# Kernel tuning notes

Hardware: AMD Instinct MI355X
Metric: run time of the kernel (lower is better)

## Reference

```python
import jax, jax.numpy as jnp
import numpy as np

EPS = 1e-5

def setup_inputs() -> dict:
    key = jax.random.key(0)
    ks = jax.random.split(key, 10)
    B, N, D = 1, 20000, 256
    E, H = 320000, 8
    s = 1.0 / np.sqrt(D)
    return {
        "node_embeddings": jax.random.normal(ks[0], (B, N, D), jnp.float32),
        "edge_index": jax.random.randint(ks[1], (2, E), 0, N, jnp.int32),
        "edge_weights": jax.random.uniform(ks[2], (E,), jnp.float32),
        "Wq": jax.random.normal(ks[3], (D, D), jnp.float32) * s,
        "Wk": jax.random.normal(ks[4], (D, D), jnp.float32) * s,
        "Wv": jax.random.normal(ks[5], (D, D), jnp.float32) * s,
        "We": jax.random.normal(ks[6], (H,), jnp.float32),  # edge_encoder weight [num_heads,1] squeezed
        "Wo": jax.random.normal(ks[7], (D, D), jnp.float32) * s,
        "ln_g": jnp.ones((D,), jnp.float32),
        "ln_b": jnp.zeros((D,), jnp.float32),
    }

def reference(node_embeddings, edge_index, edge_weights, Wq, Wk, Wv, We, Wo, ln_g, ln_b):
    B, N, D = node_embeddings.shape
    H = We.shape[0]
    hd = D // H
    scale = 1.0 / np.sqrt(hd)
    residual = node_embeddings

    # projections -> [B, N, H, hd]
    Q = (node_embeddings @ Wq).reshape(B, N, H, hd)
    K = (node_embeddings @ Wk).reshape(B, N, H, hd)
    V = (node_embeddings @ Wv).reshape(B, N, H, hd)

    src = edge_index[0]
    tgt = edge_index[1]
    E = src.shape[0]

    # gather per edge, edge axis leading for segment ops: [E, B, H, hd]
    Q_e = jnp.moveaxis(Q[:, src], 1, 0)
    K_e = jnp.moveaxis(K[:, tgt], 1, 0)
    V_e = jnp.moveaxis(V[:, tgt], 1, 0)

    # per-edge scores [E, B, H]
    scores = (Q_e * K_e).sum(-1) * scale
    bias = edge_weights[:, None] * We[None, :]            # [E, H]
    scores = scores + bias[:, None, :]

    # scatter softmax grouped by source node
    m = jax.ops.segment_max(scores, src, num_segments=N)   # [N, B, H]
    p = jnp.exp(scores - m[src])
    denom = jax.ops.segment_sum(p, src, num_segments=N)    # [N, B, H]
    attn = p / denom[src]                                   # [E, B, H]

    # scatter-add weighted V -> [N, B, H, hd]
    weighted = attn[..., None] * V_e
    agg = jax.ops.segment_sum(weighted.reshape(E, -1), src, num_segments=N)
    agg = agg.reshape(N, B, H, hd)

    attn_out = jnp.moveaxis(agg, 0, 1).reshape(B, N, D)     # [B, N, D]
    out = attn_out @ Wo

    x = out + residual
    mu = x.mean(-1, keepdims=True)
    var = ((x - mu) ** 2).mean(-1, keepdims=True)
    return (x - mu) / jnp.sqrt(var + EPS) * ln_g + ln_b
```

## Files before the change

kernel.cpp:

```cpp
#include <hip/hip_runtime.h>
#include <hip/hip_bf16.h>

typedef __attribute__((ext_vector_type(8))) short short8;
typedef __attribute__((ext_vector_type(4))) int intx4;
typedef __attribute__((ext_vector_type(2))) float floatx2;
typedef __attribute__((ext_vector_type(4))) float f32x4;

#define CH 64

__device__ __forceinline__ ushort f2b(float f) {
  __hip_bfloat16 h = __float2bfloat16(f);
  return *reinterpret_cast<ushort*>(&h);
}
__device__ __forceinline__ float b2f(ushort u) {
  return __uint_as_float(((unsigned)u) << 16);
}
__device__ __forceinline__ unsigned char f2e4(float f) {
  int p = __builtin_amdgcn_cvt_pk_fp8_f32(f, f, 0, false);
  return (unsigned char)(p & 0xff);
}
__device__ __forceinline__ void wave_lds_sync() {
  asm volatile("s_waitcnt lgkmcnt(0)" ::: "memory");
  __builtin_amdgcn_wave_barrier();
}

__global__ __launch_bounds__(256) void pre_kernel(
    const float* __restrict__ X, ushort* __restrict__ Xb, int nX,
    const float* __restrict__ Wq, const float* __restrict__ Wk,
    const float* __restrict__ Wv, const float* __restrict__ Wo,
    ushort* __restrict__ Wt, int* __restrict__ counts, int N, int nxb) {
  __shared__ float L[32][33];
  int b = blockIdx.x;
  int t = threadIdx.x;
  if (b < nxb) {
    int i = (b * 256 + t) * 8;
    if (i >= nX) return;
    float4 x0 = *reinterpret_cast<const float4*>(X + i);
    float4 x1 = *reinterpret_cast<const float4*>(X + i + 4);
    short8 o;
    o[0] = (short)f2b(x0.x); o[1] = (short)f2b(x0.y);
    o[2] = (short)f2b(x0.z); o[3] = (short)f2b(x0.w);
    o[4] = (short)f2b(x1.x); o[5] = (short)f2b(x1.y);
    o[6] = (short)f2b(x1.z); o[7] = (short)f2b(x1.w);
    *reinterpret_cast<short8*>(Xb + i) = o;
  } else if (b < nxb + 256) {
    int bx = b - nxb;
    int mat = bx >> 6;
    int tile = bx & 63;
    int tr = (tile >> 3) * 32;
    int tc = (tile & 7) * 32;
    const float* W = (mat == 0) ? Wq : (mat == 1) ? Wk : (mat == 2) ? Wv : Wo;
    int c = t & 31, r8 = t >> 5;
#pragma unroll
    for (int rr = 0; rr < 4; ++rr) {
      int r = r8 + rr * 8;
      L[r][c] = W[(size_t)(tr + r) * 256 + tc + c];
    }
    __syncthreads();
#pragma unroll
    for (int rr = 0; rr < 4; ++rr) {
      int cc = r8 + rr * 8;
      Wt[(size_t)(mat * 256 + tc + cc) * 256 + tr + c] = f2b(L[c][cc]);
    }
  } else {
    int i = (b - nxb - 256) * 256 + t;
    if (i < N) counts[i] = 0;
  }
}

__global__ __launch_bounds__(256) void gemm_hist(
    const ushort* __restrict__ Xb, const ushort* __restrict__ Wt,
    ushort* __restrict__ Qb, unsigned char* __restrict__ Kb8,
    unsigned char* __restrict__ Vb8, const int* __restrict__ src,
    int* __restrict__ counts, int N, int E, int ngemm) {
  __shared__ ushort sA[128 * 64];
  __shared__ ushort sB[128 * 64];
  int bid = blockIdx.x;
  int t = threadIdx.x;
  if (bid >= ngemm) {
    int e = (bid - ngemm) * 256 + t;
    if (e < E) atomicAdd(&counts[src[e]], 1);
    return;
  }
  int q = ngemm >> 3, r = ngemm & 7;
  int xcd = bid & 7;
  int wgid = (xcd < r ? xcd * (q + 1) : r * (q + 1) + (xcd - r) * q) + (bid >> 3);
  int bx = wgid / 6, by = wgid % 6;
  char* cA = (char*)sA;
  char* cB = (char*)sB;
  int lane = t & 63, w = t >> 6;
  int wr = w >> 1, wc = w & 1;
  int row0 = bx * 128;
  int lr = lane & 15, kg = lane >> 4;
  f32x4 acc[4][4] = {};
  for (int k0 = 0; k0 < 256; k0 += 64) {
#pragma unroll
    for (int it = 0; it < 4; ++it) {
      int slot = t + it * 256;
      int row = slot >> 3, kc = slot & 7;
      int grow = min(row0 + row, N - 1);
      short8 va = *reinterpret_cast<const short8*>(Xb + (size_t)grow * 256 + k0 + kc * 8);
      *reinterpret_cast<short8*>(cA + ((row * 128 + kc * 16) ^ ((row & 7) << 4))) = va;
      short8 vb = *reinterpret_cast<const short8*>(Wt + (size_t)(by * 128 + row) * 256 + k0 + kc * 8);
      *reinterpret_cast<short8*>(cB + ((row * 128 + kc * 16) ^ ((row & 7) << 4))) = vb;
    }
    __syncthreads();
#pragma unroll
    for (int ks = 0; ks < 2; ++ks) {
      short8 af[4], bf[4];
#pragma unroll
      for (int fr = 0; fr < 4; ++fr) {
        int row = wr * 64 + fr * 16 + lr;
        af[fr] = *reinterpret_cast<const short8*>(
            cA + ((row * 128 + ks * 64 + kg * 16) ^ ((row & 7) << 4)));
      }
#pragma unroll
      for (int fc = 0; fc < 4; ++fc) {
        int col = wc * 64 + fc * 16 + lr;
        bf[fc] = *reinterpret_cast<const short8*>(
            cB + ((col * 128 + ks * 64 + kg * 16) ^ ((col & 7) << 4)));
      }
#pragma unroll
      for (int fr = 0; fr < 4; ++fr)
#pragma unroll
        for (int fc = 0; fc < 4; ++fc)
          acc[fr][fc] = __builtin_amdgcn_mfma_f32_16x16x32_bf16(af[fr], bf[fc], acc[fr][fc], 0, 0, 0);
    }
    __syncthreads();
  }
  int orow = kg * 4;
  int mat = by >> 1;
#pragma unroll
  for (int fr = 0; fr < 4; ++fr)
#pragma unroll
    for (int fc = 0; fc < 4; ++fc)
#pragma unroll
      for (int r2 = 0; r2 < 4; ++r2) {
        int row = row0 + wr * 64 + fr * 16 + orow + r2;
        int col = (by & 1) * 128 + wc * 64 + fc * 16 + lr;
        if (row < N) {
          float v = acc[fr][fc][r2];
          if (mat == 0)      Qb[(size_t)row * 256 + col]  = f2b(v);
          else if (mat == 1) Kb8[(size_t)row * 256 + col] = f2e4(v);
          else               Vb8[(size_t)row * 256 + col] = f2e4(v);
        }
      }
}

__global__ __launch_bounds__(1024) void scan_kernel(
    const int* __restrict__ counts, int* __restrict__ offs, int* __restrict__ cursor, int N) {
  __shared__ int wsum[16];
  __shared__ int wexc[16];
  __shared__ int s_total;
  int t = threadIdx.x;
  int lane = t & 63, wv = t >> 6;
  int per = (N + 1023) >> 10;
  int b0 = t * per;
  int e0 = min(b0 + per, N);
  int sum = 0;
  for (int i = b0; i < e0; ++i) sum += counts[i];
  int x = sum;
#pragma unroll
  for (int off = 1; off < 64; off <<= 1) {
    int y = __shfl_up(x, off);
    if (lane >= off) x += y;
  }
  if (lane == 63) wsum[wv] = x;
  __syncthreads();
  if (t < 64) {
    int s = (lane < 16) ? wsum[lane] : 0;
    int xs = s;
#pragma unroll
    for (int off = 1; off < 16; off <<= 1) {
      int y = __shfl_up(xs, off);
      if (lane >= off) xs += y;
    }
    if (lane < 16) wexc[lane] = xs - s;
    if (lane == 15) s_total = xs;
  }
  __syncthreads();
  int running = wexc[wv] + (x - sum);
  for (int i = b0; i < e0; ++i) {
    int c = counts[i];
    offs[i] = running;
    cursor[i] = running;
    running += c;
  }
  if (t == 0) offs[N] = s_total;
}

__global__ void scatter_kernel(const int* __restrict__ src, const int* __restrict__ tgt,
                               const float* __restrict__ ew, int* __restrict__ cursor,
                               int2* __restrict__ ews, int E) {
  int e = blockIdx.x * blockDim.x + threadIdx.x;
  if (e < E) {
    int pos = atomicAdd(&cursor[src[e]], 1);
    ews[pos] = make_int2(tgt[e], __float_as_int(ew[e]));
  }
}

__global__ __launch_bounds__(256) void attn_kernel(
    const ushort* __restrict__ Qb, const unsigned char* __restrict__ Kb8,
    const unsigned char* __restrict__ Vb8,
    const int* __restrict__ offs, const int2* __restrict__ ews,
    const float* __restrict__ We, ushort* __restrict__ AGGb, int N) {
  __shared__ float s_p[4][CH][8];
  __shared__ int s_tgt[4][CH];
  __shared__ float s_w[4][CH];
  int t = threadIdx.x;
  int w = t >> 6;
  int l = t & 63;
  int i = blockIdx.x * 4 + w;
  if (i >= N) return;
  int e8 = l >> 3;
  int h = l & 7;
  int hacc = l >> 3;
  const float scale = 0.17677669529663687f;
  float we = We[h];

  float qf[32];
  {
    const short8* qr = reinterpret_cast<const short8*>(Qb + (size_t)i * 256 + h * 32);
#pragma unroll
    for (int d = 0; d < 4; ++d) {
      short8 qv = qr[d];
#pragma unroll
      for (int x = 0; x < 8; ++x) qf[d * 8 + x] = b2f((ushort)qv[x]);
    }
  }

  float m = -1e30f, lsum = 0.f;
  float acc0 = 0.f, acc1 = 0.f, acc2 = 0.f, acc3 = 0.f;
  int beg = offs[i], end = offs[i + 1];

  for (int base = beg; base < end; base += CH) {
    int cnt = min(CH, end - base);
    int cnt_pad = (cnt + 7) & ~7;
    {
      bool valid = l < cnt;
      int2 te = valid ? ews[base + l] : make_int2(i, 0);
      s_tgt[w][l] = te.x;
      s_w[w][l] = valid ? __int_as_float(te.y) : 0.f;
    }
    wave_lds_sync();

    float s_local[8];
#pragma unroll
    for (int it = 0; it < 8; ++it) s_local[it] = -1e30f;

    intx4 kc[2], kn[2];
    {
      const intx4* p = reinterpret_cast<const intx4*>(
          Kb8 + (size_t)s_tgt[w][e8] * 256 + h * 32);
      kc[0] = p[0]; kc[1] = p[1];
    }
    if (8 < cnt_pad) {
      const intx4* p = reinterpret_cast<const intx4*>(
          Kb8 + (size_t)s_tgt[w][8 + e8] * 256 + h * 32);
      kn[0] = p[0]; kn[1] = p[1];
    }
    float cmax = -1e30f;
#pragma unroll
    for (int it = 0; it < 8; ++it) {
      if (it * 8 >= cnt_pad) break;
      float dot = 0.f;
#pragma unroll
      for (int c = 0; c < 2; ++c)
#pragma unroll
        for (int e = 0; e < 4; ++e) {
          floatx2 lo = __builtin_amdgcn_cvt_pk_f32_fp8(kc[c][e], false);
          floatx2 hi = __builtin_amdgcn_cvt_pk_f32_fp8(kc[c][e], true);
          int b0 = c * 16 + e * 4;
          dot += qf[b0] * lo[0] + qf[b0 + 1] * lo[1] + qf[b0 + 2] * hi[0] + qf[b0 + 3] * hi[1];
        }
      int j = it * 8 + e8;
      float s = (j < cnt) ? dot * scale + s_w[w][j] * we : -1e30f;
      s_local[it] = s;
      cmax = fmaxf(cmax, s);
      kc[0] = kn[0]; kc[1] = kn[1];
      if ((it + 2) * 8 < cnt_pad) {
        const intx4* p = reinterpret_cast<const intx4*>(
            Kb8 + (size_t)s_tgt[w][(it + 2) * 8 + e8] * 256 + h * 32);
        kn[0] = p[0]; kn[1] = p[1];
      }
    }
    cmax = fmaxf(cmax, __shfl_xor(cmax, 8));
    cmax = fmaxf(cmax, __shfl_xor(cmax, 16));
    cmax = fmaxf(cmax, __shfl_xor(cmax, 32));
    float newm = fmaxf(m, cmax);
    float f = __expf(m - newm);
    float psum = 0.f;
#pragma unroll
    for (int it = 0; it < 8; ++it) {
      if (it * 8 >= cnt_pad) break;
      int j = it * 8 + e8;
      float p = __expf(s_local[it] - newm);
      s_p[w][j][h] = p;
      psum += p;
    }
    psum += __shfl_xor(psum, 8);
    psum += __shfl_xor(psum, 16);
    psum += __shfl_xor(psum, 32);
    lsum = lsum * f + psum;
    m = newm;
    float f_acc = __shfl(f, hacc);
    acc0 *= f_acc; acc1 *= f_acc; acc2 *= f_acc; acc3 *= f_acc;
    wave_lds_sync();

#pragma unroll
    for (int g = 0; g < 8; ++g) {
      if (g * 8 >= cnt_pad) break;
      float pv[8];
      int vv[8];
#pragma unroll
      for (int k = 0; k < 8; ++k) {
        int j = g * 8 + k;
        pv[k] = s_p[w][j][hacc];
        vv[k] = *reinterpret_cast<const int*>(
            Vb8 + (size_t)s_tgt[w][j] * 256 + l * 4);
      }
#pragma unroll
      for (int k = 0; k < 8; ++k) {
        floatx2 lo = __builtin_amdgcn_cvt_pk_f32_fp8(vv[k], false);
        floatx2 hi = __builtin_amdgcn_cvt_pk_f32_fp8(vv[k], true);
        acc0 += pv[k] * lo[0];
        acc1 += pv[k] * lo[1];
        acc2 += pv[k] * hi[0];
        acc3 += pv[k] * hi[1];
      }
    }
    wave_lds_sync();
  }
  float lsum_acc = __shfl(lsum, hacc);
  float rinv = (lsum_acc > 0.f) ? 1.f / lsum_acc : 0.f;
  ushort4 o = make_ushort4(f2b(acc0 * rinv), f2b(acc1 * rinv),
                           f2b(acc2 * rinv), f2b(acc3 * rinv));
  *reinterpret_cast<ushort4*>(AGGb + (size_t)i * 256 + l * 4) = o;
}

__global__ __launch_bounds__(256) void out_ln(
    const ushort* __restrict__ AGGb, const ushort* __restrict__ Wot,
    const float* __restrict__ X, const float* __restrict__ g, const float* __restrict__ bb,
    float* __restrict__ out, int N) {
  __shared__ ushort sA[64 * 64];
  __shared__ ushort sB[256 * 64];
  char* cA = (char*)sA;
  char* cB = (char*)sB;
  int t = threadIdx.x;
  int lane = t & 63, w = t >> 6;
  int row0 = blockIdx.x * 64;
  int lr = lane & 15, kg = lane >> 4;
  f32x4 acc[16] = {};
  for (int k0 = 0; k0 < 256; k0 += 64) {
#pragma unroll
    for (int it = 0; it < 2; ++it) {
      int slot = t + it * 256;
      int row = slot >> 3, kc = slot & 7;
      int grow = min(row0 + row, N - 1);
      short8 va = *reinterpret_cast<const short8*>(AGGb + (size_t)grow * 256 + k0 + kc * 8);
      *reinterpret_cast<short8*>(cA + ((row * 128 + kc * 16) ^ ((row & 7) << 4))) = va;
    }
#pragma unroll
    for (int it = 0; it < 8; ++it) {
      int slot = t + it * 256;
      int col = slot >> 3, kc = slot & 7;
      short8 vb = *reinterpret_cast<const short8*>(Wot + (size_t)col * 256 + k0 + kc * 8);
      *reinterpret_cast<short8*>(cB + ((col * 128 + kc * 16) ^ ((col & 7) << 4))) = vb;
    }
    __syncthreads();
#pragma unroll
    for (int ks = 0; ks < 2; ++ks) {
      int arow = w * 16 + lr;
      short8 a = *reinterpret_cast<const short8*>(
          cA + ((arow * 128 + ks * 64 + kg * 16) ^ ((arow & 7) << 4)));
#pragma unroll
      for (int fc = 0; fc < 16; ++fc) {
        int col = fc * 16 + lr;
        short8 b = *reinterpret_cast<const short8*>(
            cB + ((col * 128 + ks * 64 + kg * 16) ^ ((col & 7) << 4)));
        acc[fc] = __builtin_amdgcn_mfma_f32_16x16x32_bf16(a, b, acc[fc], 0, 0, 0);
      }
    }
    __syncthreads();
  }
  float g16[16], b16[16];
#pragma unroll
  for (int fc = 0; fc < 16; ++fc) {
    g16[fc] = g[fc * 16 + lr];
    b16[fc] = bb[fc * 16 + lr];
  }
#pragma unroll
  for (int r = 0; r < 4; ++r) {
    int rowl = kg * 4 + r;
    int grow = row0 + w * 16 + rowl;
    int growc = min(grow, N - 1);
    float xv[16];
    float s = 0.f, ss = 0.f;
#pragma unroll
    for (int fc = 0; fc < 16; ++fc) {
      float v = acc[fc][r] + X[(size_t)growc * 256 + fc * 16 + lr];
      xv[fc] = v;
      s += v;
      ss += v * v;
    }
    s += __shfl_xor(s, 1);  ss += __shfl_xor(ss, 1);
    s += __shfl_xor(s, 2);  ss += __shfl_xor(ss, 2);
    s += __shfl_xor(s, 4);  ss += __shfl_xor(ss, 4);
    s += __shfl_xor(s, 8);  ss += __shfl_xor(ss, 8);
    float mu = s * (1.f / 256.f);
    float var = ss * (1.f / 256.f) - mu * mu;
    float rs = rsqrtf(var + 1e-5f);
    if (grow < N) {
#pragma unroll
      for (int fc = 0; fc < 16; ++fc)
        out[(size_t)grow * 256 + fc * 16 + lr] = (xv[fc] - mu) * rs * g16[fc] + b16[fc];
    }
  }
}

extern "C" void kernel_launch(void* const* d_in, const int* in_sizes, int n_in,
                              void* d_out, int out_size, void* d_ws, size_t ws_size,
                              hipStream_t stream) {
  const float* X  = (const float*)d_in[0];
  const int* eidx = (const int*)d_in[1];
  const float* ew = (const float*)d_in[2];
  const float* Wq = (const float*)d_in[3];
  const float* Wk = (const float*)d_in[4];
  const float* Wv = (const float*)d_in[5];
  const float* We = (const float*)d_in[6];
  const float* Wo = (const float*)d_in[7];
  const float* g  = (const float*)d_in[8];
  const float* b  = (const float*)d_in[9];
  int N = in_sizes[0] / 256;
  int E = in_sizes[1] / 2;
  const int* src = eidx;
  const int* tgt = eidx + E;
  float* out = (float*)d_out;

  char* w = (char*)d_ws;
  ushort* Xb   = (ushort*)w;        w += (size_t)N * 256 * 2;
  ushort* Wt   = (ushort*)w;        w += (size_t)1024 * 256 * 2;
  ushort* Qb   = (ushort*)w;        w += (size_t)N * 256 * 2;
  unsigned char* Kb8 = (unsigned char*)w;  w += (size_t)N * 256;
  unsigned char* Vb8 = (unsigned char*)w;  w += (size_t)N * 256;
  ushort* AGGb = (ushort*)w;        w += (size_t)N * 256 * 2;
  int* counts  = (int*)w;           w += (size_t)N * 4;
  int* offs    = (int*)w;           w += (size_t)(N + 1) * 4;
  int* cursor  = (int*)w;           w += (size_t)N * 4;
  int2* ews    = (int2*)w;          w += (size_t)E * 8;
  const ushort* Wot = Wt + (size_t)768 * 256;

  int nX = N * 256;
  int nxb = (nX / 8 + 255) / 256;
  int nzero = (N + 255) / 256;
  pre_kernel<<<nxb + 256 + nzero, 256, 0, stream>>>(X, Xb, nX, Wq, Wk, Wv, Wo, Wt, counts, N, nxb);

  int ngemm = ((N + 127) / 128) * 6;
  int nhist = (E + 255) / 256;
  gemm_hist<<<ngemm + nhist, 256, 0, stream>>>(Xb, Wt, Qb, Kb8, Vb8, src, counts, N, E, ngemm);

  scan_kernel<<<1, 1024, 0, stream>>>(counts, offs, cursor, N);
  scatter_kernel<<<(E + 255) / 256, 256, 0, stream>>>(src, tgt, ew, cursor, ews, E);
  attn_kernel<<<(N + 3) / 4, 256, 0, stream>>>(Qb, Kb8, Vb8, offs, ews, We, AGGb, N);
  out_ln<<<(N + 63) / 64, 256, 0, stream>>>(AGGb, Wot, X, g, b, out, N);
}
```

Before: 147.2 us.

## Load GEMM tiles directly to LDS and move edge histogram into pre-kernel

The QKV GEMM now stages its A and B tiles with global_load_lds, writing straight from global memory into LDS. The swizzle is applied on the global source column instead of the LDS address. The source-node histogram atomics move out of the GEMM launch into the pre-processing kernel, and the counts array is zeroed with a memset. This is meant to cut register round-trips during tile loads and keep the GEMM launch free of atomic work. It adds an extra memset launch and relies on the swizzle remap reading the same layout as the fragment loads.

```diff
diff --git a/kernel.cpp b/kernel.cpp
--- a/kernel.cpp
+++ b/kernel.cpp
@@ -23,12 +23,18 @@
   asm volatile("s_waitcnt lgkmcnt(0)" ::: "memory");
   __builtin_amdgcn_wave_barrier();
 }
+__device__ __forceinline__ void gload_lds16(const void* g, void* l) {
+  __builtin_amdgcn_global_load_lds(
+      (const __attribute__((address_space(1))) void*)g,
+      (__attribute__((address_space(3))) void*)l, 16, 0, 0);
+}
 
 __global__ __launch_bounds__(256) void pre_kernel(
     const float* __restrict__ X, ushort* __restrict__ Xb, int nX,
     const float* __restrict__ Wq, const float* __restrict__ Wk,
     const float* __restrict__ Wv, const float* __restrict__ Wo,
-    ushort* __restrict__ Wt, int* __restrict__ counts, int N, int nxb) {
+    ushort* __restrict__ Wt, const int* __restrict__ src,
+    int* __restrict__ counts, int E, int nxb) {
   __shared__ float L[32][33];
   int b = blockIdx.x;
   int t = threadIdx.x;
@@ -63,25 +69,19 @@
       Wt[(size_t)(mat * 256 + tc + cc) * 256 + tr + c] = f2b(L[c][cc]);
     }
   } else {
-    int i = (b - nxb - 256) * 256 + t;
-    if (i < N) counts[i] = 0;
-  }
-}
-
-__global__ __launch_bounds__(256) void gemm_hist(
+    int e = (b - nxb - 256) * 256 + t;
+    if (e < E) atomicAdd(&counts[src[e]], 1);
+  }
+}
+
+__global__ __launch_bounds__(256) void qkv_gemm(
     const ushort* __restrict__ Xb, const ushort* __restrict__ Wt,
     ushort* __restrict__ Qb, unsigned char* __restrict__ Kb8,
-    unsigned char* __restrict__ Vb8, const int* __restrict__ src,
-    int* __restrict__ counts, int N, int E, int ngemm) {
+    unsigned char* __restrict__ Vb8, int N, int ngemm) {
   __shared__ ushort sA[128 * 64];
   __shared__ ushort sB[128 * 64];
   int bid = blockIdx.x;
   int t = threadIdx.x;
-  if (bid >= ngemm) {
-    int e = (bid - ngemm) * 256 + t;
-    if (e < E) atomicAdd(&counts[src[e]], 1);
-    return;
-  }
   int q = ngemm >> 3, r = ngemm & 7;
   int xcd = bid & 7;
   int wgid = (xcd < r ? xcd * (q + 1) : r * (q + 1) + (xcd - r) * q) + (bid >> 3);
@@ -92,18 +92,26 @@
   int wr = w >> 1, wc = w & 1;
   int row0 = bx * 128;
   int lr = lane & 15, kg = lane >> 4;
+
+  int srow = lane >> 3;
+  int skc = (lane & 7) ^ srow;
+  int garow[4], gbrow[4];
+#pragma unroll
+  for (int gi = 0; gi < 4; ++gi) {
+    int grp = w * 4 + gi;
+    garow[gi] = min(row0 + grp * 8 + srow, N - 1);
+    gbrow[gi] = by * 128 + grp * 8 + srow;
+  }
+
   f32x4 acc[4][4] = {};
   for (int k0 = 0; k0 < 256; k0 += 64) {
 #pragma unroll
-    for (int it = 0; it < 4; ++it) {
-      int slot = t + it * 256;
-      int row = slot >> 3, kc = slot & 7;
-      int grow = min(row0 + row, N - 1);
-      short8 va = *reinterpret_cast<const short8*>(Xb + (size_t)grow * 256 + k0 + kc * 8);
-      *reinterpret_cast<short8*>(cA + ((row * 128 + kc * 16) ^ ((row & 7) << 4))) = va;
-      short8 vb = *reinterpret_cast<const short8*>(Wt + (size_t)(by * 128 + row) * 256 + k0 + kc * 8);
-      *reinterpret_cast<short8*>(cB + ((row * 128 + kc * 16) ^ ((row & 7) << 4))) = vb;
-    }
+    for (int gi = 0; gi < 4; ++gi) {
+      int grp = w * 4 + gi;
+      gload_lds16(Xb + (size_t)garow[gi] * 256 + k0 + skc * 8, cA + grp * 1024);
+      gload_lds16(Wt + (size_t)gbrow[gi] * 256 + k0 + skc * 8, cB + grp * 1024);
+    }
+    asm volatile("s_waitcnt vmcnt(0)" ::: "memory");
     __syncthreads();
 #pragma unroll
     for (int ks = 0; ks < 2; ++ks) {
@@ -450,14 +458,15 @@
   int2* ews    = (int2*)w;          w += (size_t)E * 8;
   const ushort* Wot = Wt + (size_t)768 * 256;
 
+  hipMemsetAsync(counts, 0, (size_t)N * 4, stream);
+
   int nX = N * 256;
   int nxb = (nX / 8 + 255) / 256;
-  int nzero = (N + 255) / 256;
-  pre_kernel<<<nxb + 256 + nzero, 256, 0, stream>>>(X, Xb, nX, Wq, Wk, Wv, Wo, Wt, counts, N, nxb);
+  int nhist = (E + 255) / 256;
+  pre_kernel<<<nxb + 256 + nhist, 256, 0, stream>>>(X, Xb, nX, Wq, Wk, Wv, Wo, Wt, src, counts, E, nxb);
 
   int ngemm = ((N + 127) / 128) * 6;
-  int nhist = (E + 255) / 256;
-  gemm_hist<<<ngemm + nhist, 256, 0, stream>>>(Xb, Wt, Qb, Kb8, Vb8, src, counts, N, E, ngemm);
+  qkv_gemm<<<ngemm, 256, 0, stream>>>(Xb, Wt, Qb, Kb8, Vb8, N, ngemm);
 
   scan_kernel<<<1, 1024, 0, stream>>>(counts, offs, cursor, N);
   scatter_kernel<<<(E + 255) / 256, 256, 0, stream>>>(src, tgt, ew, cursor, ews, E);
```

New measurement: 158.7 us. 7.8% more time.
